# Kernel tuning notes

Hardware: AMD Instinct MI355X
Metric: run time of the kernel (lower is better)

The kernel has to match this reference:

```python
import jax, jax.numpy as jnp
import numpy as np

N, K, H, W = 4, 8, 256, 256
C, P = 32, 200000

def setup_inputs() -> dict:
    key = jax.random.key(0)
    k1, k2, k3 = jax.random.split(key, 3)
    fragments = jax.random.randint(k1, (N, K, H, W), 0, P, dtype=jnp.int64)
    alphas = jax.random.uniform(k2, (N, K, H, W), dtype=jnp.float32)
    ptclds = jax.random.normal(k3, (C, P), dtype=jnp.float32)
    return {"fragments": fragments, "alphas": alphas, "ptclds": ptclds}

def reference(fragments, alphas, ptclds):
    # fragments: (N,K,H,W) int point indices, -1 = empty slot
    # alphas:    (N,K,H,W) per-point alpha, depth-sorted along K
    # ptclds:    (C,P) per-point features
    valid = fragments >= 0
    a = jnp.where(valid, alphas, jnp.zeros((), alphas.dtype))
    # exclusive cumulative product of transmittance (1 - a) along K
    cum = jnp.cumprod(1.0 - a, axis=1)
    cum_excl = jnp.concatenate([jnp.ones_like(cum[:, :1]), cum[:, :-1]], axis=1)
    wts = a * cum_excl  # (N,K,H,W) compositing weights
    safe_idx = jnp.where(valid, fragments, 0)
    feats = ptclds.T[safe_idx]  # gather -> (N,K,H,W,C)
    images = jnp.einsum('nkhw,nkhwc->nchw', wts, feats)  # (N,C,H,W)
    return images
```

## Files before the change

### kernel.cpp

```cpp
#include <hip/hip_runtime.h>


#define N_  4
#define K_  8
#define H_  256
#define W_  256
#define C_  32
#define P_  200000
#define HW_ (H_ * W_)

__global__ __launch_bounds__(256) void transpose_ptclds_kernel(
    const float* __restrict__ src,
    float*       __restrict__ dst)
{
    __shared__ float tile[32][33];
    const int p0 = blockIdx.x * 32;
    const int tx = threadIdx.x;
    const int ty = threadIdx.y;

#pragma unroll
    for (int r = 0; r < 4; ++r) {
        const int c = ty + r * 8;
        tile[c][tx] = src[(size_t)c * P_ + p0 + tx];
    }
    __syncthreads();
#pragma unroll
    for (int r = 0; r < 4; ++r) {
        const int pl = ty + r * 8;
        dst[(size_t)(p0 + pl) * C_ + tx] = tile[tx][pl];
    }
}

template <bool TRANSPOSED>
__global__ __launch_bounds__(256) void composite_kernel(
    const int*   __restrict__ frags,
    const float* __restrict__ alphas,
    const float* __restrict__ pt,
    float*       __restrict__ out)
{
    const int tid = blockIdx.x * blockDim.x + threadIdx.x;
    const int n  = tid >> 16;
    const int hw = tid & (HW_ - 1);
    const int base = n * K_ * HW_ + hw;

    int   idx[K_];
    float al[K_];
#pragma unroll
    for (int k = 0; k < K_; ++k) idx[k] = frags[base + k * HW_];
#pragma unroll
    for (int k = 0; k < K_; ++k) al[k] = alphas[base + k * HW_];

    float w[K_];
    float T = 1.0f;
#pragma unroll
    for (int k = 0; k < K_; ++k) {
        const bool valid = idx[k] >= 0;
        const float a = valid ? al[k] : 0.0f;
        w[k] = a * T;
        T *= (1.0f - a);
        if (!valid) idx[k] = 0;
    }

    float4 acc[8];
#pragma unroll
    for (int i = 0; i < 8; ++i) acc[i] = make_float4(0.f, 0.f, 0.f, 0.f);

    if (TRANSPOSED) {
#pragma unroll
        for (int k = 0; k < K_; ++k) {
            const float4* f =
                reinterpret_cast<const float4*>(pt + (size_t)idx[k] * C_);
            const float wk = w[k];
#pragma unroll
            for (int i = 0; i < 8; ++i) {
                const float4 v = f[i];
                acc[i].x += wk * v.x;
                acc[i].y += wk * v.y;
                acc[i].z += wk * v.z;
                acc[i].w += wk * v.w;
            }
        }
    } else {
        float* accf = reinterpret_cast<float*>(acc);
#pragma unroll
        for (int k = 0; k < K_; ++k) {
            const float wk = w[k];
#pragma unroll
            for (int c = 0; c < C_; ++c) {
                accf[c] += wk * pt[(size_t)c * P_ + idx[k]];
            }
        }
    }

    const float* accf = reinterpret_cast<const float*>(acc);
    const size_t obase = (size_t)n * C_ * HW_ + hw;
#pragma unroll
    for (int c = 0; c < C_; ++c) {
        out[obase + (size_t)c * HW_] = accf[c];
    }
}

extern "C" void kernel_launch(void* const* d_in, const int* in_sizes, int n_in,
                              void* d_out, int out_size, void* d_ws, size_t ws_size,
                              hipStream_t stream)
{
    const int*   frags  = (const int*)  d_in[0];
    const float* alphas = (const float*)d_in[1];
    const float* ptclds = (const float*)d_in[2];
    float*       out    = (float*)      d_out;

    const size_t needed = (size_t)P_ * C_ * sizeof(float);

    const int total_px  = N_ * HW_;
    const int cblocks   = total_px / 256;

    if (ws_size >= needed) {
        float* ptT = (float*)d_ws;
        dim3 tb(32, 8);
        transpose_ptclds_kernel<<<P_ / 32, tb, 0, stream>>>(ptclds, ptT);
        composite_kernel<true><<<cblocks, 256, 0, stream>>>(frags, alphas, ptT, out);
    } else {
        composite_kernel<false><<<cblocks, 256, 0, stream>>>(frags, alphas, ptclds, out);
    }
}
```

Measured before the change: 148.4 us.

## Split each pixel across eight threads by channel group and vectorize transpose

The compositing kernel now assigns one float4 channel group per thread, so eight threads cooperate on each pixel instead of one thread computing all 32 channels. This is meant to cut per-thread register use, raise occupancy and coalesce the gathers of transposed feature rows. In exchange, alpha and fragment loads and weight computation are repeated eight times per pixel, and output stores become more scattered. The transpose kernel is reworked to use 64-point tiles with float4 global loads and stores.

Result: faster. 128.8 us (-13.2%).

```diff
diff --git a/kernel.cpp b/kernel.cpp
--- a/kernel.cpp
+++ b/kernel.cpp
@@ -13,21 +13,35 @@
     const float* __restrict__ src,
     float*       __restrict__ dst)
 {
-    __shared__ float tile[32][33];
-    const int p0 = blockIdx.x * 32;
-    const int tx = threadIdx.x;
-    const int ty = threadIdx.y;
+    __shared__ float tile[32][65];
+    const int p0 = blockIdx.x * 64;
+    const int t  = threadIdx.x;
 
 #pragma unroll
-    for (int r = 0; r < 4; ++r) {
-        const int c = ty + r * 8;
-        tile[c][tx] = src[(size_t)c * P_ + p0 + tx];
+    for (int i = 0; i < 2; ++i) {
+        const int e  = i * 256 + t;
+        const int c  = e >> 4;
+        const int pg = e & 15;
+        const float4 v = *reinterpret_cast<const float4*>(
+            src + (size_t)c * P_ + p0 + pg * 4);
+        tile[c][pg * 4 + 0] = v.x;
+        tile[c][pg * 4 + 1] = v.y;
+        tile[c][pg * 4 + 2] = v.z;
+        tile[c][pg * 4 + 3] = v.w;
     }
     __syncthreads();
+
 #pragma unroll
-    for (int r = 0; r < 4; ++r) {
-        const int pl = ty + r * 8;
-        dst[(size_t)(p0 + pl) * C_ + tx] = tile[tx][pl];
+    for (int i = 0; i < 2; ++i) {
+        const int e  = i * 256 + t;
+        const int p  = e >> 3;
+        const int cc = e & 7;
+        float4 v;
+        v.x = tile[cc * 4 + 0][p];
+        v.y = tile[cc * 4 + 1][p];
+        v.z = tile[cc * 4 + 2][p];
+        v.w = tile[cc * 4 + 3][p];
+        *reinterpret_cast<float4*>(dst + (size_t)(p0 + p) * C_ + cc * 4) = v;
     }
 }
 
@@ -39,8 +53,10 @@
     float*       __restrict__ out)
 {
     const int tid = blockIdx.x * blockDim.x + threadIdx.x;
-    const int n  = tid >> 16;
-    const int hw = tid & (HW_ - 1);
+    const int gid = tid >> 3;
+    const int cg  = tid & 7;
+    const int n   = gid >> 16;
+    const int hw  = gid & (HW_ - 1);
     const int base = n * K_ * HW_ + hw;
 
     int   idx[K_];
@@ -61,43 +77,38 @@
         if (!valid) idx[k] = 0;
     }
 
-    float4 acc[8];
-#pragma unroll
-    for (int i = 0; i < 8; ++i) acc[i] = make_float4(0.f, 0.f, 0.f, 0.f);
+    float4 acc = make_float4(0.f, 0.f, 0.f, 0.f);
 
     if (TRANSPOSED) {
 #pragma unroll
         for (int k = 0; k < K_; ++k) {
-            const float4* f =
-                reinterpret_cast<const float4*>(pt + (size_t)idx[k] * C_);
+            const float4 v = *reinterpret_cast<const float4*>(
+                pt + (size_t)idx[k] * C_ + cg * 4);
             const float wk = w[k];
-#pragma unroll
-            for (int i = 0; i < 8; ++i) {
-                const float4 v = f[i];
-                acc[i].x += wk * v.x;
-                acc[i].y += wk * v.y;
-                acc[i].z += wk * v.z;
-                acc[i].w += wk * v.w;
-            }
+            acc.x += wk * v.x;
+            acc.y += wk * v.y;
+            acc.z += wk * v.z;
+            acc.w += wk * v.w;
         }
     } else {
-        float* accf = reinterpret_cast<float*>(acc);
 #pragma unroll
         for (int k = 0; k < K_; ++k) {
             const float wk = w[k];
 #pragma unroll
-            for (int c = 0; c < C_; ++c) {
-                accf[c] += wk * pt[(size_t)c * P_ + idx[k]];
+            for (int j = 0; j < 4; ++j) {
+                acc.x = (j == 0) ? acc.x + wk * pt[(size_t)(cg * 4 + 0) * P_ + idx[k]] : acc.x;
             }
+            acc.y += wk * pt[(size_t)(cg * 4 + 1) * P_ + idx[k]];
+            acc.z += wk * pt[(size_t)(cg * 4 + 2) * P_ + idx[k]];
+            acc.w += wk * pt[(size_t)(cg * 4 + 3) * P_ + idx[k]];
         }
     }
 
-    const float* accf = reinterpret_cast<const float*>(acc);
     const size_t obase = (size_t)n * C_ * HW_ + hw;
-#pragma unroll
-    for (int c = 0; c < C_; ++c) {
-        out[obase + (size_t)c * HW_] = accf[c];
-    }
+    out[obase + (size_t)(cg * 4 + 0) * HW_] = acc.x;
+    out[obase + (size_t)(cg * 4 + 1) * HW_] = acc.y;
+    out[obase + (size_t)(cg * 4 + 2) * HW_] = acc.z;
+    out[obase + (size_t)(cg * 4 + 3) * HW_] = acc.w;
 }
 
 extern "C" void kernel_launch(void* const* d_in, const int* in_sizes, int n_in,
@@ -111,13 +122,12 @@
 
     const size_t needed = (size_t)P_ * C_ * sizeof(float);
 
-    const int total_px  = N_ * HW_;
-    const int cblocks   = total_px / 256;
+    const int total_thr = N_ * HW_ * 8;
+    const int cblocks   = total_thr / 256;
 
     if (ws_size >= needed) {
         float* ptT = (float*)d_ws;
-        dim3 tb(32, 8);
-        transpose_ptclds_kernel<<<P_ / 32, tb, 0, stream>>>(ptclds, ptT);
+        transpose_ptclds_kernel<<<P_ / 64, 256, 0, stream>>>(ptclds, ptT);
         composite_kernel<true><<<cblocks, 256, 0, stream>>>(frags, alphas, ptT, out);
     } else {
         composite_kernel<false><<<cblocks, 256, 0, stream>>>(frags, alphas, ptclds, out);
```
